# Optimization experiments

Measured on AMD Instinct MI355X. Metric: run time of the kernel, lower is better.

The kernel has to match this reference:

```python
import jax, jax.numpy as jnp
import numpy as np

K = 64                      # sort-pool k
B_GRAPHS, N_PER = 256, 512  # graphs, nodes per graph
DIM_F, E_PER = 128, 8192    # node feature dim, edges per graph
EMB = 32


def setup_inputs() -> dict:
    key = jax.random.key(0)
    ks = jax.random.split(key, 12)
    N = B_GRAPHS * N_PER
    off = (jnp.arange(B_GRAPHS) * N_PER)[:, None]
    x = jax.random.normal(ks[0], (N, DIM_F), jnp.float32)
    edge_src = (jax.random.randint(ks[1], (B_GRAPHS, E_PER), 0, N_PER) + off).reshape(-1)
    edge_dst = (jax.random.randint(ks[2], (B_GRAPHS, E_PER), 0, N_PER) + off).reshape(-1)

    def lin(k, o, i):
        return (jax.random.normal(k, (o, i), jnp.float32) / np.float32(np.sqrt(i)))

    return {
        "x": x,
        "W0": lin(ks[3], EMB, DIM_F), "b0": jnp.zeros((EMB,), jnp.float32),
        "W1": lin(ks[4], EMB, EMB),   "b1": jnp.zeros((EMB,), jnp.float32),
        "W2": lin(ks[5], EMB, EMB),   "b2": jnp.zeros((EMB,), jnp.float32),
        "W3": lin(ks[6], 1, EMB),     "b3": jnp.zeros((1,), jnp.float32),
        "conv1_w": jax.random.normal(ks[7], (16, 1, 97), jnp.float32) / np.float32(np.sqrt(97.0)),
        "conv1_b": jnp.zeros((16,), jnp.float32),
        "conv2_w": jax.random.normal(ks[8], (32, 16, 5), jnp.float32) / np.float32(np.sqrt(80.0)),
        "conv2_b": jnp.zeros((32,), jnp.float32),
        "d1_w": lin(ks[9], 128, 896),  "d1_b": jnp.zeros((128,), jnp.float32),
        "d2_w": lin(ks[10], 10, 128),  "d2_b": jnp.zeros((10,), jnp.float32),
        "edge_src": edge_src, "edge_dst": edge_dst,
        "num_graphs": B_GRAPHS,
    }


def _dgcnn_conv(h_in, W, b, src, dst):
    # h = lin(x); message = (1/deg_src)[dst] * h[src]; scatter-add at dst
    N = h_in.shape[0]
    h = h_in @ W.T + b
    deg = jax.ops.segment_sum(jnp.ones_like(src, dtype=h.dtype), src, num_segments=N)
    norm = 1.0 / deg                       # self-loops guarantee deg >= 1
    msg = h[src] * norm[dst][:, None]      # [E+N, C]
    return jax.ops.segment_sum(msg, dst, num_segments=N)


def _forward(x, W0, b0, W1, b1, W2, b2, W3, b3,
             conv1_w, conv1_b, conv2_w, conv2_b,
             d1_w, d1_b, d2_w, d2_b, src, dst, num_graphs):
    N = x.shape[0]
    self_idx = jnp.arange(N)
    src = jnp.concatenate([src, self_idx])   # add_self_loops
    dst = jnp.concatenate([dst, self_idx])
    hs = []
    h = x
    for (W, b) in ((W0, b0), (W1, b1), (W2, b2), (W3, b3)):
        h = jnp.tanh(_dgcnn_conv(h, W, b, src, dst))
        hs.append(h)
    feat = jnp.concatenate(hs, axis=1)       # [N, 97]
    D = feat.shape[1]
    B = num_graphs
    n = N // B
    g = feat.reshape(B, n, D)
    # global_sort_pool: sort nodes per graph by last channel, descending, take top-k
    order = jnp.argsort(-g[:, :, -1], axis=1)[:, :K]
    topk = jnp.take_along_axis(g, order[:, :, None], axis=1)   # [B, K, D]
    # Conv1d(1,16,kernel=D,stride=D) over [B,1,K*D] == per-node linear on D
    c1 = jax.nn.relu(jnp.einsum('bkd,od->bok', topk, conv1_w[:, 0, :])
                     + conv1_b[None, :, None])                  # [B,16,K]
    p = c1.reshape(B, 16, K // 2, 2).max(axis=-1)               # MaxPool1d(2,2)
    c2 = jax.lax.conv_general_dilated(p, conv2_w, (1,), 'VALID',
                                      dimension_numbers=('NCH', 'OIH', 'NCH'))
    c2 = jax.nn.relu(c2 + conv2_b[None, :, None])               # [B,32,28]
    flat = c2.reshape(B, -1)                                    # [B,896]
    hid = jax.nn.relu(flat @ d1_w.T + d1_b)                     # dropout = identity (eval)
    return hid @ d2_w.T + d2_b                                  # [B,10]


def reference(x, W0, b0, W1, b1, W2, b2, W3, b3,
              conv1_w, conv1_b, conv2_w, conv2_b,
              d1_w, d1_b, d2_w, d2_b, edge_src, edge_dst, num_graphs):
    return _forward(x, W0, b0, W1, b1, W2, b2, W3, b3,
                    conv1_w, conv1_b, conv2_w, conv2_b,
                    d1_w, d1_b, d2_w, d2_b, edge_src, edge_dst, num_graphs)
```

## Files before the change

kernel.cpp:

```cpp
#include <hip/hip_runtime.h>

#define NG   256
#define NP   512
#define EPG  8192
#define FDIM 128
#define STB  36

#define OFF_STAGE 0
#define OFF_BUFB  65536
#define OFF_CSR   139264
#define OFF_OFFS  155648
#define OFF_WT    156680
#define OFF_CUR   156712
#define OFF_DCNT  158760
#define OFF_NRM   160808
#define SMEM_SZ   162856

#define OFF_KEY   OFF_CSR
#define OFF_RANKP (OFF_CSR + 2048)
#define OFF_TIDX  (OFF_CSR + 4096)
#define OFF_TKEY  (OFF_CSR + 4352)
#define OFF_L3    OFF_CUR
#define FO_FEAT 0
#define FO_C1   6208
#define FO_P    7232
#define FO_C2   7744
#define FO_HID  8640

__global__ __launch_bounds__(1024, 4) void dgcnn_fused(
    const float* __restrict__ x,
    const float* __restrict__ W0, const float* __restrict__ b0,
    const float* __restrict__ W1, const float* __restrict__ b1,
    const float* __restrict__ W2, const float* __restrict__ b2,
    const float* __restrict__ W3, const float* __restrict__ b3,
    const float* __restrict__ c1w, const float* __restrict__ c1b,
    const float* __restrict__ c2w, const float* __restrict__ c2b,
    const float* __restrict__ d1w, const float* __restrict__ d1b,
    const float* __restrict__ d2w, const float* __restrict__ d2b,
    const int* __restrict__ esrc, const int* __restrict__ edst,
    float* __restrict__ hs2,
    float* __restrict__ out)
{
  extern __shared__ char smem[];
  float*          stageF = (float*)(smem + OFF_STAGE);
  float*          bufB  = (float*)(smem + OFF_BUFB);
  unsigned short* csr   = (unsigned short*)(smem + OFF_CSR);
  unsigned short* offs  = (unsigned short*)(smem + OFF_OFFS);
  unsigned int*   wt    = (unsigned int*)(smem + OFF_WT);
  unsigned int*   cur   = (unsigned int*)(smem + OFF_CUR);
  unsigned int*   dcnt  = (unsigned int*)(smem + OFF_DCNT);
  float*          nrm   = (float*)(smem + OFF_NRM);
  float*          lin3S = (float*)(smem + OFF_L3);
  float*          keyA  = (float*)(smem + OFF_KEY);
  unsigned short* rankP = (unsigned short*)(smem + OFF_RANKP);
  unsigned short* topIdx= (unsigned short*)(smem + OFF_TIDX);
  float*          topKey= (float*)(smem + OFF_TKEY);

  const int g    = blockIdx.x;
  const int tid  = threadIdx.x;
  const int lane = tid & 63;
  const int wv   = __builtin_amdgcn_readfirstlane(tid >> 6);
  const int half = __builtin_amdgcn_readfirstlane(tid >> 9);
  const int v    = tid & 511;
  const int nb   = g * NP;

  const int ldRow0 = tid >> 3;
  const int ldGrp  = tid & 7;
  const int ldSwz  = (ldGrp ^ (ldRow0 & 7)) * 16;
  auto load_chunk = [&](int kc, float4* xr) {
    const float* base = x + (size_t)nb * FDIM + kc * 32 + ldGrp * 4;
#pragma unroll
    for (int it = 0; it < 4; it++)
      xr[it] = *(const float4*)(base + (size_t)(ldRow0 + it * 128) * FDIM);
  };
  auto store_chunk = [&](const float4* xr) {
#pragma unroll
    for (int it = 0; it < 4; it++)
      *(float4*)(smem + OFF_STAGE + (ldRow0 + it * 128) * 128 + ldSwz) = xr[it];
  };

  const int eb = g * EPG;
  const int4* s4p = (const int4*)(esrc + eb);
  const int4* d4p = (const int4*)(edst + eb);
  const int4 sa = s4p[tid], sb = s4p[tid + 1024];
  const int4 da = d4p[tid], db = d4p[tid + 1024];
  float4 xr[4], xr2[4];
  load_chunk(0, xr);

  if (tid < 512) { cur[tid] = 0u; dcnt[tid] = 0u; }
  __syncthreads();

  int es[8], ed[8];
  {
    es[0]=sa.x-nb; es[1]=sa.y-nb; es[2]=sa.z-nb; es[3]=sa.w-nb;
    es[4]=sb.x-nb; es[5]=sb.y-nb; es[6]=sb.z-nb; es[7]=sb.w-nb;
    ed[0]=da.x-nb; ed[1]=da.y-nb; ed[2]=da.z-nb; ed[3]=da.w-nb;
    ed[4]=db.x-nb; ed[5]=db.y-nb; ed[6]=db.z-nb; ed[7]=db.w-nb;
#pragma unroll
    for (int i = 0; i < 8; i++) {
      atomicAdd(&dcnt[es[i]], 1u);
      atomicAdd(&dcnt[ed[i]], 65536u);
    }
  }
  __syncthreads();

  unsigned c_scan = 0;
  if (tid < 512) {
    const unsigned cw = dcnt[tid];
    nrm[tid] = 1.0f / (float)((cw & 0xFFFFu) + 1u);
    c_scan = cw >> 16;
    for (int d = 1; d < 64; d <<= 1) {
      const unsigned t = __shfl_up(c_scan, (unsigned)d, 64);
      if (lane >= d) c_scan += t;
    }
    if (lane == 63) wt[wv] = c_scan;
  }
  __syncthreads();
  if (tid < 512) {
    unsigned base = 0;
    for (int w = 0; w < wv; w++) base += wt[w];
    offs[tid + 1] = (unsigned short)(base + c_scan);
    if (tid == 0) offs[0] = 0;
  }
  __syncthreads();

#pragma unroll
  for (int i = 0; i < 8; i++) {
    const unsigned pos = (unsigned)offs[ed[i]] + atomicAdd(&cur[ed[i]], 1u);
    csr[pos] = (unsigned short)es[i];
  }

  float acc0[16];
#pragma unroll
  for (int c = 0; c < 16; c++) acc0[c] = b0[half * 16 + c];
  const char* rowp = smem + OFF_STAGE + v * 128;
  const int vswz = v & 7;
  for (int kc = 0; kc < 4; kc++) {
    __syncthreads();
    store_chunk(xr);
    if (kc < 3) load_chunk(kc + 1, xr2);
    __syncthreads();
#pragma unroll
    for (int jg = 0; jg < 8; jg++) {
      const float4 t = *(const float4*)(rowp + ((jg ^ vswz) * 16));
#pragma unroll
      for (int c = 0; c < 16; c++) {
        const float* wr = W0 + (size_t)(half * 16 + c) * FDIM + kc * 32 + jg * 4;
        acc0[c] = fmaf(t.x, wr[0], acc0[c]);
        acc0[c] = fmaf(t.y, wr[1], acc0[c]);
        acc0[c] = fmaf(t.z, wr[2], acc0[c]);
        acc0[c] = fmaf(t.w, wr[3], acc0[c]);
      }
    }
#pragma unroll
    for (int it = 0; it < 4; it++) xr[it] = xr2[it];
  }
  {
    float4* br = (float4*)(bufB + v * STB + half * 16);
#pragma unroll
    for (int j = 0; j < 4; j++)
      br[j] = make_float4(acc0[j*4+0], acc0[j*4+1], acc0[j*4+2], acc0[j*4+3]);
  }
  __syncthreads();

  float h[16];
  auto do_agg = [&]() {
    float4 A0, A1, A2, A3;
    const float4* sr = (const float4*)(bufB + v * STB + half * 16);
    A0 = sr[0]; A1 = sr[1]; A2 = sr[2]; A3 = sr[3];
    const int e0 = offs[v], e1 = offs[v + 1];
    int e = e0;
    for (; e + 1 < e1; e += 2) {
      const int s0 = csr[e], s1 = csr[e + 1];
      const float4* rb0 = (const float4*)(bufB + s0 * STB + half * 16);
      const float4* rb1 = (const float4*)(bufB + s1 * STB + half * 16);
      const float4 p0 = rb0[0], p1 = rb0[1], p2 = rb0[2], p3 = rb0[3];
      const float4 q0 = rb1[0], q1 = rb1[1], q2 = rb1[2], q3 = rb1[3];
      A0.x += p0.x + q0.x; A0.y += p0.y + q0.y; A0.z += p0.z + q0.z; A0.w += p0.w + q0.w;
      A1.x += p1.x + q1.x; A1.y += p1.y + q1.y; A1.z += p1.z + q1.z; A1.w += p1.w + q1.w;
      A2.x += p2.x + q2.x; A2.y += p2.y + q2.y; A2.z += p2.z + q2.z; A2.w += p2.w + q2.w;
      A3.x += p3.x + q3.x; A3.y += p3.y + q3.y; A3.z += p3.z + q3.z; A3.w += p3.w + q3.w;
    }
    if (e < e1) {
      const int s = csr[e];
      const float4* rb = (const float4*)(bufB + s * STB + half * 16);
      const float4 r0 = rb[0], r1 = rb[1], r2 = rb[2], r3 = rb[3];
      A0.x += r0.x; A0.y += r0.y; A0.z += r0.z; A0.w += r0.w;
      A1.x += r1.x; A1.y += r1.y; A1.z += r1.z; A1.w += r1.w;
      A2.x += r2.x; A2.y += r2.y; A2.z += r2.z; A2.w += r2.w;
      A3.x += r3.x; A3.y += r3.y; A3.z += r3.z; A3.w += r3.w;
    }
    const float nv = nrm[v];
    h[0]=tanhf(A0.x*nv); h[1]=tanhf(A0.y*nv); h[2]=tanhf(A0.z*nv); h[3]=tanhf(A0.w*nv);
    h[4]=tanhf(A1.x*nv); h[5]=tanhf(A1.y*nv); h[6]=tanhf(A1.z*nv); h[7]=tanhf(A1.w*nv);
    h[8]=tanhf(A2.x*nv); h[9]=tanhf(A2.y*nv); h[10]=tanhf(A2.z*nv); h[11]=tanhf(A2.w*nv);
    h[12]=tanhf(A3.x*nv); h[13]=tanhf(A3.y*nv); h[14]=tanhf(A3.z*nv); h[15]=tanhf(A3.w*nv);
  };

  auto put_h = [&]() {
    float4* br = (float4*)(bufB + v * STB + half * 16);
#pragma unroll
    for (int j = 0; j < 4; j++)
      br[j] = make_float4(h[j*4+0], h[j*4+1], h[j*4+2], h[j*4+3]);
  };

  auto store_h1 = [&]() {
#pragma unroll
    for (int c = 0; c < 16; c++)
      stageF[(half * 16 + c) * 512 + v] = h[c];
  };

  auto spill2 = [&]() {
    float4* dst = (float4*)(hs2 + (size_t)(nb + v) * 32 + half * 16);
#pragma unroll
    for (int j = 0; j < 4; j++)
      dst[j] = make_float4(h[j*4+0], h[j*4+1], h[j*4+2], h[j*4+3]);
  };

  auto do_lin = [&](const float* __restrict__ W, const float* __restrict__ b) {
    float hf[32];
    const float4* rr = (const float4*)(bufB + v * STB);
#pragma unroll
    for (int j = 0; j < 8; j++) {
      const float4 t = rr[j];
      hf[j*4+0]=t.x; hf[j*4+1]=t.y; hf[j*4+2]=t.z; hf[j*4+3]=t.w;
    }
    __syncthreads();
    float acc[16];
#pragma unroll
    for (int c = 0; c < 16; c++) {
      const int C = half * 16 + c;
      const float* wr = W + C * 32;
      float a = b[C];
#pragma unroll
      for (int j = 0; j < 32; j++) a = fmaf(hf[j], wr[j], a);
      acc[c] = a;
    }
    float4* br = (float4*)(bufB + v * STB + half * 16);
#pragma unroll
    for (int j = 0; j < 4; j++)
      br[j] = make_float4(acc[j*4+0], acc[j*4+1], acc[j*4+2], acc[j*4+3]);
    __syncthreads();
  };

  do_agg();
  __syncthreads();
  put_h(); store_h1();
  __syncthreads();
  do_lin(W1, b1);
  do_agg();
  __syncthreads();
  put_h(); spill2();
  __syncthreads();
  do_lin(W2, b2);
  do_agg();
  __syncthreads();
  put_h();
  __syncthreads();

  if (tid < 512) {
    const float4* rr = (const float4*)(bufB + tid * STB);
    double a = (double)b3[0];
#pragma unroll
    for (int j = 0; j < 8; j++) {
      const float4 t = rr[j];
      a = fma((double)t.x, (double)W3[j*4+0], a);
      a = fma((double)t.y, (double)W3[j*4+1], a);
      a = fma((double)t.z, (double)W3[j*4+2], a);
      a = fma((double)t.w, (double)W3[j*4+3], a);
    }
    lin3S[tid] = (float)a;
  }
  __syncthreads();
  float h4 = 0.f;
  if (tid < 512) {
    double a = (double)lin3S[tid];
    const int e0 = offs[tid], e1 = offs[tid + 1];
    for (int e = e0; e < e1; e++) a += (double)lin3S[csr[e]];
    a *= (double)nrm[tid];
    h4 = tanhf((float)a);
  }
  __syncthreads();
  if (tid < 512) keyA[tid] = h4;
  __syncthreads();

  {
    const int i = tid & 511;
    const int p = tid >> 9;
    const float ki = keyA[i];
    const float4* k4 = (const float4*)(keyA + p * 256);
    int cnt = 0;
#pragma unroll 8
    for (int jj = 0; jj < 64; jj++) {
      const float4 kv = k4[jj];
      const int j0 = p * 256 + jj * 4;
      cnt += (kv.x > ki || (kv.x == ki && (j0    ) < i)) ? 1 : 0;
      cnt += (kv.y > ki || (kv.y == ki && (j0 + 1) < i)) ? 1 : 0;
      cnt += (kv.z > ki || (kv.z == ki && (j0 + 2) < i)) ? 1 : 0;
      cnt += (kv.w > ki || (kv.w == ki && (j0 + 3) < i)) ? 1 : 0;
    }
    rankP[tid] = (unsigned short)cnt;
  }
  __syncthreads();
  if (tid < 512) {
    const int r = (int)rankP[tid] + (int)rankP[tid + 512];
    if (r < 64) { topIdx[r] = (unsigned short)tid; topKey[r] = keyA[tid]; }
  }
  __syncthreads();

  {
    const int k = lane;
    const int t = wv;
    const int node = (int)topIdx[k];
    const float a0 = stageF[ t       * 512 + node];
    const float a1 = stageF[(t + 16) * 512 + node];
    const float* h2row = hs2 + (size_t)(nb + node) * 32;
    const float b0v = h2row[t];
    const float b1v = h2row[t + 16];
    const float* brow = bufB + node * STB;
    const float c0v = brow[t];
    const float c1v = brow[t + 16];
    const float kk = topKey[k];
    __syncthreads();
    float* featS = bufB + FO_FEAT;
    featS[ t        * 64 + k] = a0;
    featS[(t + 16)  * 64 + k] = a1;
    featS[(t + 32)  * 64 + k] = b0v;
    featS[(t + 48)  * 64 + k] = b1v;
    featS[(t + 64)  * 64 + k] = c0v;
    featS[(t + 80)  * 64 + k] = c1v;
    if (t == 0) featS[96 * 64 + k] = kk;
  }
  __syncthreads();

  {
    const float* featS = bufB + FO_FEAT;
    float* c1s = bufB + FO_C1;
    const int ch = wv;
    double a = (double)c1b[ch];
    const float* wr = c1w + ch * 97;
    for (int d = 0; d < 97; d++)
      a = fma((double)featS[d * 64 + lane], (double)wr[d], a);
    c1s[ch * 64 + lane] = fmaxf((float)a, 0.f);
  }
  __syncthreads();

  if (tid < 512) {
    const float* c1s = bufB + FO_C1;
    float* ps  = bufB + FO_P;
    const int o = tid >> 5, jj = tid & 31;
    ps[o * 32 + jj] = fmaxf(c1s[o * 64 + 2 * jj], c1s[o * 64 + 2 * jj + 1]);
  }
  __syncthreads();

  {
    const float* ps  = bufB + FO_P;
    float* c2s = bufB + FO_C2;
    const int o = wv;
    if (lane < 28) {
      double a0 = 0., a1 = 0.;
      for (int i = 0; i < 16; i++) {
#pragma unroll
        for (int r = 0; r < 5; r++) {
          const double pv = (double)ps[i * 32 + lane + r];
          a0 = fma(pv, (double)c2w[((o     ) * 16 + i) * 5 + r], a0);
          a1 = fma(pv, (double)c2w[((o + 16) * 16 + i) * 5 + r], a1);
        }
      }
      c2s[(o     ) * 28 + lane] = fmaxf((float)(a0 + (double)c2b[o     ]), 0.f);
      c2s[(o + 16) * 28 + lane] = fmaxf((float)(a1 + (double)c2b[o + 16]), 0.f);
    }
  }
  __syncthreads();

  {
    const float* c2s  = bufB + FO_C2;
    float* hids = bufB + FO_HID;
    float fl[14];
#pragma unroll
    for (int j = 0; j < 14; j++) fl[j] = c2s[lane + j * 64];
    for (int hh = 0; hh < 8; hh++) {
      const int hI = wv * 8 + hh;
      const float* wr = d1w + (size_t)hI * 896;
      double a = 0.;
#pragma unroll
      for (int j = 0; j < 14; j++) a = fma((double)fl[j], (double)wr[lane + j * 64], a);
#pragma unroll
      for (int m = 32; m > 0; m >>= 1) a += __shfl_xor(a, m, 64);
      if (lane == 0) hids[hI] = fmaxf((float)(a + (double)d1b[hI]), 0.f);
    }
  }
  __syncthreads();

  if (tid < 10) {
    const float* hids = bufB + FO_HID;
    const float* wr = d2w + tid * 128;
    double a = (double)d2b[tid];
#pragma unroll 8
    for (int hh = 0; hh < 128; hh++) a = fma((double)hids[hh], (double)wr[hh], a);
    out[g * 10 + tid] = (float)a;
  }
}

extern "C" void kernel_launch(void* const* d_in, const int* in_sizes, int n_in,
                              void* d_out, int out_size, void* d_ws, size_t ws_size,
                              hipStream_t stream) {
  const float* x   = (const float*)d_in[0];
  const float* W0  = (const float*)d_in[1];
  const float* b0  = (const float*)d_in[2];
  const float* W1  = (const float*)d_in[3];
  const float* b1  = (const float*)d_in[4];
  const float* W2  = (const float*)d_in[5];
  const float* b2  = (const float*)d_in[6];
  const float* W3  = (const float*)d_in[7];
  const float* b3  = (const float*)d_in[8];
  const float* c1w = (const float*)d_in[9];
  const float* c1b = (const float*)d_in[10];
  const float* c2w = (const float*)d_in[11];
  const float* c2b = (const float*)d_in[12];
  const float* d1w = (const float*)d_in[13];
  const float* d1b = (const float*)d_in[14];
  const float* d2w = (const float*)d_in[15];
  const float* d2b = (const float*)d_in[16];
  const int* esrc  = (const int*)d_in[17];
  const int* edst  = (const int*)d_in[18];

  float* hs2 = (float*)d_ws;
  float* outp = (float*)d_out;

  hipFuncSetAttribute(reinterpret_cast<const void*>(dgcnn_fused),
                      hipFuncAttributeMaxDynamicSharedMemorySize, SMEM_SZ);
  dgcnn_fused<<<NG, 1024, SMEM_SZ, stream>>>(x, W0, b0, W1, b1, W2, b2, W3, b3,
                                             c1w, c1b, c2w, c2b, d1w, d1b, d2w, d2b,
                                             esrc, edst, hs2, outp);
}
```

Before: 285.4 us.

## Interleave CSR build with linear-layer chunks, unroll aggregation, use fp32 in head

The degree counting, prefix scan, offset computation and CSR scatter are spread across the four K-chunks of the first linear layer, so the phases share barriers and overlap with the GEMM work instead of running as a separate serial prologue. The neighbour aggregation loop gets a 4-way unrolled body to expose more shared-memory loads at once. The conv1, conv2 and dense-layer accumulations switch from double to float FMA, removing slow FP64 arithmetic and conversions. The fp32 switch may change rounding slightly relative to the reference, and the interleaved schedule depends on the barrier ordering being correct.

```diff
diff --git a/kernel.cpp b/kernel.cpp
--- a/kernel.cpp
+++ b/kernel.cpp
@@ -79,67 +79,29 @@
       *(float4*)(smem + OFF_STAGE + (ldRow0 + it * 128) * 128 + ldSwz) = xr[it];
   };
 
+  float4 xr[4], xr2[4];
+  load_chunk(0, xr);
   const int eb = g * EPG;
   const int4* s4p = (const int4*)(esrc + eb);
   const int4* d4p = (const int4*)(edst + eb);
   const int4 sa = s4p[tid], sb = s4p[tid + 1024];
   const int4 da = d4p[tid], db = d4p[tid + 1024];
-  float4 xr[4], xr2[4];
-  load_chunk(0, xr);
+
+  int es[8], ed[8];
+  es[0]=sa.x-nb; es[1]=sa.y-nb; es[2]=sa.z-nb; es[3]=sa.w-nb;
+  es[4]=sb.x-nb; es[5]=sb.y-nb; es[6]=sb.z-nb; es[7]=sb.w-nb;
+  ed[0]=da.x-nb; ed[1]=da.y-nb; ed[2]=da.z-nb; ed[3]=da.w-nb;
+  ed[4]=db.x-nb; ed[5]=db.y-nb; ed[6]=db.z-nb; ed[7]=db.w-nb;
 
   if (tid < 512) { cur[tid] = 0u; dcnt[tid] = 0u; }
-  __syncthreads();
-
-  int es[8], ed[8];
-  {
-    es[0]=sa.x-nb; es[1]=sa.y-nb; es[2]=sa.z-nb; es[3]=sa.w-nb;
-    es[4]=sb.x-nb; es[5]=sb.y-nb; es[6]=sb.z-nb; es[7]=sb.w-nb;
-    ed[0]=da.x-nb; ed[1]=da.y-nb; ed[2]=da.z-nb; ed[3]=da.w-nb;
-    ed[4]=db.x-nb; ed[5]=db.y-nb; ed[6]=db.z-nb; ed[7]=db.w-nb;
-#pragma unroll
-    for (int i = 0; i < 8; i++) {
-      atomicAdd(&dcnt[es[i]], 1u);
-      atomicAdd(&dcnt[ed[i]], 65536u);
-    }
-  }
-  __syncthreads();
-
-  unsigned c_scan = 0;
-  if (tid < 512) {
-    const unsigned cw = dcnt[tid];
-    nrm[tid] = 1.0f / (float)((cw & 0xFFFFu) + 1u);
-    c_scan = cw >> 16;
-    for (int d = 1; d < 64; d <<= 1) {
-      const unsigned t = __shfl_up(c_scan, (unsigned)d, 64);
-      if (lane >= d) c_scan += t;
-    }
-    if (lane == 63) wt[wv] = c_scan;
-  }
-  __syncthreads();
-  if (tid < 512) {
-    unsigned base = 0;
-    for (int w = 0; w < wv; w++) base += wt[w];
-    offs[tid + 1] = (unsigned short)(base + c_scan);
-    if (tid == 0) offs[0] = 0;
-  }
-  __syncthreads();
-
-#pragma unroll
-  for (int i = 0; i < 8; i++) {
-    const unsigned pos = (unsigned)offs[ed[i]] + atomicAdd(&cur[ed[i]], 1u);
-    csr[pos] = (unsigned short)es[i];
-  }
 
   float acc0[16];
 #pragma unroll
   for (int c = 0; c < 16; c++) acc0[c] = b0[half * 16 + c];
   const char* rowp = smem + OFF_STAGE + v * 128;
   const int vswz = v & 7;
-  for (int kc = 0; kc < 4; kc++) {
-    __syncthreads();
-    store_chunk(xr);
-    if (kc < 3) load_chunk(kc + 1, xr2);
-    __syncthreads();
+
+  auto compute_chunk = [&](const int kc) {
 #pragma unroll
     for (int jg = 0; jg < 8; jg++) {
       const float4 t = *(const float4*)(rowp + ((jg ^ vswz) * 16));
@@ -152,9 +114,58 @@
         acc0[c] = fmaf(t.w, wr[3], acc0[c]);
       }
     }
-#pragma unroll
-    for (int it = 0; it < 4; it++) xr[it] = xr2[it];
-  }
+  };
+
+  __syncthreads();
+  store_chunk(xr);
+  load_chunk(1, xr2);
+  __syncthreads();
+#pragma unroll
+  for (int i = 0; i < 8; i++) {
+    atomicAdd(&dcnt[es[i]], 1u);
+    atomicAdd(&dcnt[ed[i]], 65536u);
+  }
+  compute_chunk(0);
+#pragma unroll
+  for (int it = 0; it < 4; it++) xr[it] = xr2[it];
+  __syncthreads();
+  store_chunk(xr);
+  load_chunk(2, xr2);
+  __syncthreads();
+  unsigned c_scan = 0;
+  if (tid < 512) {
+    const unsigned cw = dcnt[tid];
+    nrm[tid] = 1.0f / (float)((cw & 0xFFFFu) + 1u);
+    c_scan = cw >> 16;
+    for (int d = 1; d < 64; d <<= 1) {
+      const unsigned t = __shfl_up(c_scan, (unsigned)d, 64);
+      if (lane >= d) c_scan += t;
+    }
+    if (lane == 63) wt[wv] = c_scan;
+  }
+  compute_chunk(1);
+#pragma unroll
+  for (int it = 0; it < 4; it++) xr[it] = xr2[it];
+  __syncthreads();
+  store_chunk(xr);
+  load_chunk(3, xr2);
+  __syncthreads();
+  if (tid < 512) {
+    unsigned base = 0;
+    for (int w = 0; w < wv; w++) base += wt[w];
+    offs[tid + 1] = (unsigned short)(base + c_scan);
+    if (tid == 0) offs[0] = 0;
+  }
+  compute_chunk(2);
+  __syncthreads();
+  store_chunk(xr2);
+  __syncthreads();
+#pragma unroll
+  for (int i = 0; i < 8; i++) {
+    const unsigned pos = (unsigned)offs[ed[i]] + atomicAdd(&cur[ed[i]], 1u);
+    csr[pos] = (unsigned short)es[i];
+  }
+  compute_chunk(3);
   {
     float4* br = (float4*)(bufB + v * STB + half * 16);
 #pragma unroll
@@ -170,6 +181,25 @@
     A0 = sr[0]; A1 = sr[1]; A2 = sr[2]; A3 = sr[3];
     const int e0 = offs[v], e1 = offs[v + 1];
     int e = e0;
+    for (; e + 3 < e1; e += 4) {
+      const int s0 = csr[e], s1 = csr[e + 1], s2 = csr[e + 2], s3 = csr[e + 3];
+      const float4* rb0 = (const float4*)(bufB + s0 * STB + half * 16);
+      const float4* rb1 = (const float4*)(bufB + s1 * STB + half * 16);
+      const float4* rb2 = (const float4*)(bufB + s2 * STB + half * 16);
+      const float4* rb3 = (const float4*)(bufB + s3 * STB + half * 16);
+      const float4 p0 = rb0[0], p1 = rb0[1], p2 = rb0[2], p3 = rb0[3];
+      const float4 q0 = rb1[0], q1 = rb1[1], q2 = rb1[2], q3 = rb1[3];
+      const float4 r0 = rb2[0], r1 = rb2[1], r2 = rb2[2], r3 = rb2[3];
+      const float4 t0 = rb3[0], t1 = rb3[1], t2 = rb3[2], t3 = rb3[3];
+      A0.x += p0.x + q0.x; A0.y += p0.y + q0.y; A0.z += p0.z + q0.z; A0.w += p0.w + q0.w;
+      A1.x += p1.x + q1.x; A1.y += p1.y + q1.y; A1.z += p1.z + q1.z; A1.w += p1.w + q1.w;
+      A2.x += p2.x + q2.x; A2.y += p2.y + q2.y; A2.z += p2.z + q2.z; A2.w += p2.w + q2.w;
+      A3.x += p3.x + q3.x; A3.y += p3.y + q3.y; A3.z += p3.z + q3.z; A3.w += p3.w + q3.w;
+      A0.x += r0.x + t0.x; A0.y += r0.y + t0.y; A0.z += r0.z + t0.z; A0.w += r0.w + t0.w;
+      A1.x += r1.x + t1.x; A1.y += r1.y + t1.y; A1.z += r1.z + t1.z; A1.w += r1.w + t1.w;
+      A2.x += r2.x + t2.x; A2.y += r2.y + t2.y; A2.z += r2.z + t2.z; A2.w += r2.w + t2.w;
+      A3.x += r3.x + t3.x; A3.y += r3.y + t3.y; A3.z += r3.z + t3.z; A3.w += r3.w + t3.w;
+    }
     for (; e + 1 < e1; e += 2) {
       const int s0 = csr[e], s1 = csr[e + 1];
       const float4* rb0 = (const float4*)(bufB + s0 * STB + half * 16);
@@ -337,11 +367,11 @@
     const float* featS = bufB + FO_FEAT;
     float* c1s = bufB + FO_C1;
     const int ch = wv;
-    double a = (double)c1b[ch];
+    float a = c1b[ch];
     const float* wr = c1w + ch * 97;
     for (int d = 0; d < 97; d++)
-      a = fma((double)featS[d * 64 + lane], (double)wr[d], a);
-    c1s[ch * 64 + lane] = fmaxf((float)a, 0.f);
+      a = fmaf(featS[d * 64 + lane], wr[d], a);
+    c1s[ch * 64 + lane] = fmaxf(a, 0.f);
   }
   __syncthreads();
 
@@ -358,17 +388,17 @@
     float* c2s = bufB + FO_C2;
     const int o = wv;
     if (lane < 28) {
-      double a0 = 0., a1 = 0.;
+      float a0 = 0.f, a1 = 0.f;
       for (int i = 0; i < 16; i++) {
 #pragma unroll
         for (int r = 0; r < 5; r++) {
-          const double pv = (double)ps[i * 32 + lane + r];
-          a0 = fma(pv, (double)c2w[((o     ) * 16 + i) * 5 + r], a0);
-          a1 = fma(pv, (double)c2w[((o + 16) * 16 + i) * 5 + r], a1);
+          const float pv = ps[i * 32 + lane + r];
+          a0 = fmaf(pv, c2w[((o     ) * 16 + i) * 5 + r], a0);
+          a1 = fmaf(pv, c2w[((o + 16) * 16 + i) * 5 + r], a1);
         }
       }
-      c2s[(o     ) * 28 + lane] = fmaxf((float)(a0 + (double)c2b[o     ]), 0.f);
-      c2s[(o + 16) * 28 + lane] = fmaxf((float)(a1 + (double)c2b[o + 16]), 0.f);
+      c2s[(o     ) * 28 + lane] = fmaxf(a0 + c2b[o     ], 0.f);
+      c2s[(o + 16) * 28 + lane] = fmaxf(a1 + c2b[o + 16], 0.f);
     }
   }
   __syncthreads();
@@ -379,15 +409,16 @@
     float fl[14];
 #pragma unroll
     for (int j = 0; j < 14; j++) fl[j] = c2s[lane + j * 64];
+#pragma unroll 2
     for (int hh = 0; hh < 8; hh++) {
       const int hI = wv * 8 + hh;
       const float* wr = d1w + (size_t)hI * 896;
-      double a = 0.;
-#pragma unroll
-      for (int j = 0; j < 14; j++) a = fma((double)fl[j], (double)wr[lane + j * 64], a);
+      float a = 0.f;
+#pragma unroll
+      for (int j = 0; j < 14; j++) a = fmaf(fl[j], wr[lane + j * 64], a);
 #pragma unroll
       for (int m = 32; m > 0; m >>= 1) a += __shfl_xor(a, m, 64);
-      if (lane == 0) hids[hI] = fmaxf((float)(a + (double)d1b[hI]), 0.f);
+      if (lane == 0) hids[hI] = fmaxf(a + d1b[hI], 0.f);
     }
   }
   __syncthreads();
```

Measured after the change: 281.2 us. No clear change (-1.5%).
